# Kernel tuning notes

Measured on AMD Instinct MI355X. Metric: run time of the kernel, lower is better.

Reference implementation:

```python
import jax, jax.numpy as jnp
import numpy as np

B, S, H, L = 256, 128, 1024, 2
FEATS = {"t": 300, "v": 35, "a": 74}


def setup_inputs() -> dict:
    key = jax.random.key(0)
    inp = {}
    k = 0

    def nk():
        nonlocal k
        k += 1
        return jax.random.fold_in(key, k)

    inp["t_input"] = jax.random.normal(nk(), (B, S, FEATS["t"]), jnp.float32)
    inp["v_input"] = jax.random.normal(nk(), (B, S, FEATS["v"]), jnp.float32)
    inp["a_input"] = jax.random.normal(nk(), (B, S, FEATS["a"]), jnp.float32)
    std = 1.0 / np.sqrt(H)
    for m, f in FEATS.items():
        in_sizes = [f + 2 * H, H]  # layer0 gets modality feat + two cross-modal hiddens
        for l in range(L):
            inp[f"Wih_{m}{l}"] = jax.random.normal(nk(), (4 * H, in_sizes[l]), jnp.float32) * std
            inp[f"Whh_{m}{l}"] = jax.random.normal(nk(), (4 * H, H), jnp.float32) * std
            inp[f"bih_{m}{l}"] = jax.random.normal(nk(), (4 * H,), jnp.float32) * std
            inp[f"bhh_{m}{l}"] = jax.random.normal(nk(), (4 * H,), jnp.float32) * std
    inp["Wd"] = jax.random.normal(nk(), (1, 3 * H), jnp.float32) * np.sqrt(2.0 / (1 + 3 * H))
    inp["bd"] = jnp.zeros((1,), jnp.float32)
    return inp


def _cell(x, h, c, Wih, Whh, bih, bhh):
    # PyTorch LSTM gate order: i, f, g, o
    z = x @ Wih.T + h @ Whh.T + bih + bhh  # [B, 4H]
    i, f, g, o = jnp.split(z, 4, axis=-1)
    c_new = jax.nn.sigmoid(f) * c + jax.nn.sigmoid(i) * jnp.tanh(g)
    h_new = jax.nn.sigmoid(o) * jnp.tanh(c_new)
    return h_new, c_new


def _stack_cell(x, hs, cs, layers):
    new_h, new_c = [], []
    inp = x
    for l, (Wih, Whh, bih, bhh) in enumerate(layers):
        h, c = _cell(inp, hs[l], cs[l], Wih, Whh, bih, bhh)
        new_h.append(h)
        new_c.append(c)
        inp = h
    return jnp.stack(new_h), jnp.stack(new_c)


def _forward(t_input, v_input, a_input, pt, pv, pa, Wd, bd):
    z = jnp.zeros((L, B, H), t_input.dtype)
    carry0 = (z, z, z, z, z, z)
    xs = (t_input.transpose(1, 0, 2), v_input.transpose(1, 0, 2), a_input.transpose(1, 0, 2))

    def step(carry, x):
        ht, ct, hv, cv, ha, ca = carry
        xt, xv, xa = x
        tf, vf, af = ht[-1], hv[-1], ha[-1]  # top-layer hiddens from previous step
        t_in = jnp.concatenate([xt, vf, af], axis=-1)
        v_in = jnp.concatenate([xv, tf, af], axis=-1)
        a_in = jnp.concatenate([xa, tf, vf], axis=-1)
        ht, ct = _stack_cell(t_in, ht, ct, pt)
        hv, cv = _stack_cell(v_in, hv, cv, pv)
        ha, ca = _stack_cell(a_in, ha, ca, pa)
        return (ht, ct, hv, cv, ha, ca), None

    (ht, ct, hv, cv, ha, ca), _ = jax.lax.scan(step, carry0, xs)
    feat = jnp.concatenate([ht[-1], hv[-1], ha[-1]], axis=-1)  # [B, 3H]
    return feat @ Wd.T + bd  # [B, 1]


def reference(t_input, v_input, a_input,
              Wih_t0, Whh_t0, bih_t0, bhh_t0, Wih_t1, Whh_t1, bih_t1, bhh_t1,
              Wih_v0, Whh_v0, bih_v0, bhh_v0, Wih_v1, Whh_v1, bih_v1, bhh_v1,
              Wih_a0, Whh_a0, bih_a0, bhh_a0, Wih_a1, Whh_a1, bih_a1, bhh_a1,
              Wd, bd):
    pt = [(Wih_t0, Whh_t0, bih_t0, bhh_t0), (Wih_t1, Whh_t1, bih_t1, bhh_t1)]
    pv = [(Wih_v0, Whh_v0, bih_v0, bhh_v0), (Wih_v1, Whh_v1, bih_v1, bhh_v1)]
    pa = [(Wih_a0, Whh_a0, bih_a0, bhh_a0), (Wih_a1, Whh_a1, bih_a1, bhh_a1)]
    return _forward(t_input, v_input, a_input, pt, pv, pa, Wd, bd)
```

## Files before the change

### kernel.cpp

```cpp
#include <hip/hip_runtime.h>
#include <hip/hip_fp16.h>
#include <cstdint>
#include <cstddef>


typedef _Float16 half8 __attribute__((ext_vector_type(8)));
typedef float floatx4 __attribute__((ext_vector_type(4)));

__device__ __forceinline__ void gload16(const void* g, void* l) {
  __builtin_amdgcn_global_load_lds(
      (const __attribute__((address_space(1))) void*)g,
      (__attribute__((address_space(3))) void*)l, 16, 0, 0);
}
__device__ __forceinline__ float fsig(float x) {
  return 1.f / (1.f + __expf(-x));
}
__device__ __forceinline__ float ftanhf(float x) {
  x = fminf(15.f, fmaxf(-15.f, x));
  float e = __expf(2.f * x);
  return (e - 1.f) / (e + 1.f);
}

struct ModParam {
  const __half* xseg;
  const __half* inseg;
  const __half* W;
  const float* bias;
  float* c;
  __half* dst0; __half* dst1; __half* dst2;
  int off0, off1, off2;
  __half* feat; int featoff;
  int Kx, Kin;
};
struct PhaseParams { ModParam m[3]; };

__global__ __launch_bounds__(256, 3) void lstm_phase(PhaseParams P) {
  const int b_ = blockIdx.x;
  const int xcd = b_ & 7, rnd = b_ >> 3;
  const int pairIdx = xcd * 24 + (rnd >> 2);
  const int mt = rnd & 3;
  const int mod = pairIdx >> 6;
  const int bn = pairIdx & 63;
  const ModParam p = P.m[mod];
  const int nKt = (p.Kx + p.Kin) >> 7;
  const int KxT = p.Kx >> 7;
  const int tid = threadIdx.x;
  const int lane = tid & 63, wid = tid >> 6;
  const int ln = lane & 15, lm = lane >> 4, c4 = lane & 3;

  __shared__ __align__(16) __half smem[3][1024][8];

  floatx4 acc[4][4];
#pragma unroll
  for (int a = 0; a < 4; ++a)
#pragma unroll
    for (int b = 0; b < 4; ++b) acc[a][b] = (floatx4)0.f;

  half8 bvA[4], bvB[4];

  auto stageA = [&](int kt, int buf) {
    const __half* base; int kq0;
    if (kt < KxT) { base = p.xseg;  kq0 = kt * 16; }
    else          { base = p.inseg; kq0 = (kt - KxT) * 16; }
#pragma unroll
    for (int it = 0; it < 4; ++it) {
      int idx = it * 256 + tid;
      int kql = idx >> 6, bl = idx & 63;
      gload16(base + ((size_t)(kq0 + kql) * 256 + mt * 64 + bl) * 8,
              &smem[buf][idx][0]);
    }
  };
  auto loadB = [&](int kt, half8 (&bv)[4]) {
    const __half* src =
        p.W + ((size_t)(bn * nKt + kt) * 4 + wid) * 2048 + lane * 8;
#pragma unroll
    for (int ni = 0; ni < 4; ++ni) bv[ni] = *(const half8*)(src + ni * 512);
  };
  auto compute = [&](int buf, const half8 (&bv)[4]) {
    half8 av[4];
    const int kq = wid * 4 + lm;
#pragma unroll
    for (int mi = 0; mi < 4; ++mi)
      av[mi] = *(const half8*)&smem[buf][kq * 64 + mi * 16 + ln][0];
#pragma unroll
    for (int mi = 0; mi < 4; ++mi)
#pragma unroll
      for (int ni = 0; ni < 4; ++ni)
        acc[mi][ni] = __builtin_amdgcn_mfma_f32_16x16x32_f16(
            av[mi], bv[ni], acc[mi][ni], 0, 0, 0);
  };

  stageA(0, 0);
  loadB(0, bvA);
  int kt = 0;
  while (true) {
    if (kt + 1 < nKt) {
      stageA(kt + 1, (kt + 1) % 3);
      loadB(kt + 1, bvB);
      asm volatile("s_waitcnt vmcnt(8)" ::: "memory");
    } else {
      asm volatile("s_waitcnt vmcnt(0)" ::: "memory");
    }
    __builtin_amdgcn_s_barrier();
    __builtin_amdgcn_sched_barrier(0);
    compute(kt % 3, bvA);
    if (++kt >= nKt) break;
    if (kt + 1 < nKt) {
      stageA(kt + 1, (kt + 1) % 3);
      loadB(kt + 1, bvA);
      asm volatile("s_waitcnt vmcnt(8)" ::: "memory");
    } else {
      asm volatile("s_waitcnt vmcnt(0)" ::: "memory");
    }
    __builtin_amdgcn_s_barrier();
    __builtin_amdgcn_sched_barrier(0);
    compute(kt % 3, bvB);
    if (++kt >= nKt) break;
  }
  __syncthreads();

  floatx4* rbuf = (floatx4*)&smem[0][0][0];
  auto slot = [&](int h, int ni, int w) {
    return ((h * 4 + ni) * 4 + w) * 64 + lane;
  };
  floatx4 own[4];
#pragma unroll
  for (int ni = 0; ni < 4; ++ni) {
    rbuf[slot(0, ni, wid)] = acc[0][ni];
    rbuf[slot(1, ni, wid)] = acc[1][ni];
  }
  __syncthreads();
  if (wid == 0) {
#pragma unroll
    for (int ni = 0; ni < 4; ++ni)
      own[ni] = acc[0][ni] + rbuf[slot(0, ni, 1)] + rbuf[slot(0, ni, 2)] +
                rbuf[slot(0, ni, 3)];
  } else if (wid == 1) {
#pragma unroll
    for (int ni = 0; ni < 4; ++ni)
      own[ni] = acc[1][ni] + rbuf[slot(1, ni, 0)] + rbuf[slot(1, ni, 2)] +
                rbuf[slot(1, ni, 3)];
  }
  __syncthreads();
#pragma unroll
  for (int ni = 0; ni < 4; ++ni) {
    rbuf[slot(0, ni, wid)] = acc[2][ni];
    rbuf[slot(1, ni, wid)] = acc[3][ni];
  }
  __syncthreads();
  if (wid == 2) {
#pragma unroll
    for (int ni = 0; ni < 4; ++ni)
      own[ni] = acc[2][ni] + rbuf[slot(0, ni, 0)] + rbuf[slot(0, ni, 1)] +
                rbuf[slot(0, ni, 3)];
  } else if (wid == 3) {
#pragma unroll
    for (int ni = 0; ni < 4; ++ni)
      own[ni] = acc[3][ni] + rbuf[slot(1, ni, 0)] + rbuf[slot(1, ni, 1)] +
                rbuf[slot(1, ni, 2)];
  }

#pragma unroll
  for (int ni = 0; ni < 4; ++ni) {
    const int ncol = bn * 64 + ni * 16 + ln;
    const float bia = p.bias[ncol];
    const int j = ncol >> 2;
#pragma unroll
    for (int r = 0; r < 4; ++r) {
      float v = own[ni][r] + bia;
      float g1 = __shfl_xor(v, 1);
      float g2 = __shfl_xor(v, 2);
      float g3 = __shfl_xor(v, 3);
      int m0 = c4, m1 = c4 ^ 1, m2 = c4 ^ 2, m3 = c4 ^ 3;
      float zi = m0 == 0 ? v : (m0 == 1 ? g1 : (m0 == 2 ? g2 : g3));
      float zf = m1 == 0 ? v : (m1 == 1 ? g1 : (m1 == 2 ? g2 : g3));
      float zg = m2 == 0 ? v : (m2 == 1 ? g1 : (m2 == 2 ? g2 : g3));
      float zo = m3 == 0 ? v : (m3 == 1 ? g1 : (m3 == 2 ? g2 : g3));
      const int b = mt * 64 + wid * 16 + lm * 4 + r;
      float cp = p.c[b * 1024 + j];
      float cn = fsig(zf) * cp + fsig(zi) * ftanhf(zg);
      float hn = fsig(zo) * ftanhf(cn);
      __half h16 = __float2half(hn);
      if (c4 == 0) {
        if (p.dst0) {
          int col = p.off0 + j;
          p.dst0[(size_t)(col >> 3) * 2048 + b * 8 + (col & 7)] = h16;
        }
      } else if (c4 == 1) {
        if (p.dst1) {
          int col = p.off1 + j;
          p.dst1[(size_t)(col >> 3) * 2048 + b * 8 + (col & 7)] = h16;
        }
      } else if (c4 == 2) {
        if (p.dst2) {
          int col = p.off2 + j;
          p.dst2[(size_t)(col >> 3) * 2048 + b * 8 + (col & 7)] = h16;
        }
      } else {
        p.c[b * 1024 + j] = cn;
        if (p.feat) p.feat[(size_t)b * 3072 + p.featoff + j] = h16;
      }
    }
  }
}

__global__ void pack_w(__half* dst, const float* Wih, const float* Whh,
                       float* bdst, const float* bih, const float* bhh,
                       int f, int fpad, int hih, int Ktot) {
  long long i = (long long)blockIdx.x * 256 + threadIdx.x;
  long long tot = (long long)4096 * Ktot;
  const int nKt = Ktot >> 7;
  if (i < tot) {
    int q = (int)(i >> 11);
    int wid = q & 3;
    int p2 = q >> 2;
    int ktile = p2 % nKt, nt = p2 / nKt;
    int r = (int)(i & 2047);
    int ni = r >> 9, lane = (r >> 3) & 63, e = r & 7;
    int n = nt * 64 + ni * 16 + (lane & 15);
    int nsrc = (n & 3) * 1024 + (n >> 2);
    int k = ktile * 128 + wid * 32 + (lane >> 4) * 8 + e;
    float v;
    if (k < fpad)
      v = (k < f) ? Wih[(size_t)nsrc * (f + hih) + k] : 0.f;
    else if (k < fpad + hih)
      v = Wih[(size_t)nsrc * (f + hih) + f + (k - fpad)];
    else
      v = Whh[(size_t)nsrc * 1024 + (k - fpad - hih)];
    dst[i] = __float2half(v);
  }
  if (i < 4096) {
    int nsrc = ((int)i & 3) * 1024 + ((int)i >> 2);
    bdst[i] = bih[nsrc] + bhh[nsrc];
  }
}

__global__ void pack_x(__half* dst, const float* x, int f, int fpad) {
  long long i = (long long)blockIdx.x * 256 + threadIdx.x;
  long long tot = (long long)128 * 256 * fpad;
  if (i >= tot) return;
  int e = (int)(i & 7);
  long long u = i >> 3;
  int b = (int)(u & 255);
  long long v = u >> 8;
  int nq = fpad >> 3;
  int kq = (int)(v % nq);
  int t = (int)(v / nq);
  int k = kq * 8 + e;
  dst[i] = (k < f) ? __float2half(x[((size_t)b * 128 + t) * f + k])
                   : __float2half(0.f);
}

__global__ void final_dot(const __half* feat, const float* Wd, const float* bd,
                          float* out) {
  int b = blockIdx.x, tid = threadIdx.x;
  float s = 0.f;
  for (int j = tid; j < 3072; j += 256)
    s += __half2float(feat[(size_t)b * 3072 + j]) * Wd[j];
  __shared__ float red[256];
  red[tid] = s;
  __syncthreads();
  for (int o = 128; o > 0; o >>= 1) {
    if (tid < o) red[tid] += red[tid + o];
    __syncthreads();
  }
  if (tid == 0) out[b] = red[0] + bd[0];
}

extern "C" void kernel_launch(void* const* d_in, const int* in_sizes, int n_in,
                              void* d_out, int out_size, void* d_ws, size_t ws_size,
                              hipStream_t stream) {
  const int B = 256, S = 128, H = 1024, NG = 4096;
  const int FRAW[3] = {300, 35, 74};
  const int FPAD[3] = {384, 128, 128};

  const float* xin[3] = {(const float*)d_in[0], (const float*)d_in[1],
                         (const float*)d_in[2]};
  const float *Wih0[3], *Whh0[3], *bih0[3], *bhh0[3];
  const float *Wih1[3], *Whh1[3], *bih1[3], *bhh1[3];
  for (int m = 0; m < 3; ++m) {
    int bidx = 3 + m * 8;
    Wih0[m] = (const float*)d_in[bidx + 0];
    Whh0[m] = (const float*)d_in[bidx + 1];
    bih0[m] = (const float*)d_in[bidx + 2];
    bhh0[m] = (const float*)d_in[bidx + 3];
    Wih1[m] = (const float*)d_in[bidx + 4];
    Whh1[m] = (const float*)d_in[bidx + 5];
    bih1[m] = (const float*)d_in[bidx + 6];
    bhh1[m] = (const float*)d_in[bidx + 7];
  }
  const float* Wd = (const float*)d_in[27];
  const float* bd = (const float*)d_in[28];

  uint8_t* wsb = (uint8_t*)d_ws;
  size_t off = 0;
  auto alloc = [&](size_t bytes) -> void* {
    void* p = wsb + off;
    off += (bytes + 255) & ~(size_t)255;
    return p;
  };

  __half* W0[3];
  __half* W1[3];
  int K0[3];
  for (int m = 0; m < 3; ++m) {
    K0[m] = FPAD[m] + 3 * H;
    W0[m] = (__half*)alloc((size_t)NG * K0[m] * 2);
  }
  for (int m = 0; m < 3; ++m) W1[m] = (__half*)alloc((size_t)NG * 2 * H * 2);
  float* biasB = (float*)alloc((size_t)6 * NG * 4);
  __half* X16[3];
  for (int m = 0; m < 3; ++m)
    X16[m] = (__half*)alloc((size_t)S * B * FPAD[m] * 2);
  size_t stateStart = off;
  __half* In0[3];
  __half* In1[3];
  for (int m = 0; m < 3; ++m) In0[m] = (__half*)alloc((size_t)2 * B * 3072 * 2);
  for (int m = 0; m < 3; ++m) In1[m] = (__half*)alloc((size_t)2 * B * 2048 * 2);
  float* cbuf = (float*)alloc((size_t)6 * B * H * 4);
  size_t stateEnd = off;
  __half* featB = (__half*)alloc((size_t)B * 3072 * 2);

  if (off > ws_size) return;

  for (int m = 0; m < 3; ++m) {
    long long tot0 = (long long)NG * K0[m];
    pack_w<<<dim3((unsigned)((tot0 + 255) / 256)), 256, 0, stream>>>(
        W0[m], Wih0[m], Whh0[m], biasB + m * NG, bih0[m], bhh0[m],
        FRAW[m], FPAD[m], 2 * H, K0[m]);
    long long tot1 = (long long)NG * 2 * H;
    pack_w<<<dim3((unsigned)((tot1 + 255) / 256)), 256, 0, stream>>>(
        W1[m], Wih1[m], Whh1[m], biasB + (3 + m) * NG, bih1[m], bhh1[m],
        0, 0, H, 2 * H);
    long long totx = (long long)S * B * FPAD[m];
    pack_x<<<dim3((unsigned)((totx + 255) / 256)), 256, 0, stream>>>(
        X16[m], xin[m], FRAW[m], FPAD[m]);
  }
  hipMemsetAsync(wsb + stateStart, 0, stateEnd - stateStart, stream);

  for (int t = 0; t < S; ++t) {
    int pq = t & 1;
    __half* in0cur[3], *in0nxt[3], *in1cur[3], *in1nxt[3];
    for (int m = 0; m < 3; ++m) {
      in0cur[m] = In0[m] + (size_t)pq * B * 3072;
      in0nxt[m] = In0[m] + (size_t)(pq ^ 1) * B * 3072;
      in1cur[m] = In1[m] + (size_t)pq * B * 2048;
      in1nxt[m] = In1[m] + (size_t)(pq ^ 1) * B * 2048;
    }

    PhaseParams PA;
    for (int m = 0; m < 3; ++m) {
      ModParam& q = PA.m[m];
      q.xseg = X16[m] + (size_t)t * B * FPAD[m];
      q.Kx = FPAD[m];
      q.inseg = in0cur[m];
      q.Kin = 3072;
      q.W = W0[m];
      q.bias = biasB + m * NG;
      q.c = cbuf + (size_t)m * B * H;
      q.dst0 = in1cur[m]; q.off0 = 0;
      q.dst1 = in0nxt[m]; q.off1 = 2048;
      q.dst2 = nullptr;   q.off2 = 0;
      q.feat = nullptr;   q.featoff = 0;
    }
    lstm_phase<<<dim3(768), 256, 0, stream>>>(PA);

    PhaseParams PB;
    for (int m = 0; m < 3; ++m) {
      ModParam& q = PB.m[m];
      q.xseg = nullptr; q.Kx = 0;
      q.inseg = in1cur[m]; q.Kin = 2048;
      q.W = W1[m];
      q.bias = biasB + (3 + m) * NG;
      q.c = cbuf + (size_t)(3 + m) * B * H;
      q.feat = (t == S - 1) ? featB : nullptr;
      q.featoff = m * H;
      if (m == 0) {
        q.dst0 = in0nxt[1]; q.off0 = 0;
        q.dst1 = in0nxt[2]; q.off1 = 0;
        q.dst2 = in1nxt[0]; q.off2 = 1024;
      } else if (m == 1) {
        q.dst0 = in0nxt[0]; q.off0 = 0;
        q.dst1 = in0nxt[2]; q.off1 = 1024;
        q.dst2 = in1nxt[1]; q.off2 = 1024;
      } else {
        q.dst0 = in0nxt[0]; q.off0 = 1024;
        q.dst1 = in0nxt[1]; q.off1 = 1024;
        q.dst2 = in1nxt[2]; q.off2 = 1024;
      }
    }
    lstm_phase<<<dim3(768), 256, 0, stream>>>(PB);
  }

  final_dot<<<dim3(256), 256, 0, stream>>>(featB, Wd, bd, (float*)d_out);
}
```

Baseline: 9.882 ms.

## Give each wave a private LDS A-slice and drop per-tile block barriers

Rearranges the shared-memory A tile so each wave loads, with global_load_lds, exactly the K rows it later reads. That makes the per-k-tile s_barrier unnecessary, since waves no longer consume data written by other waves. It also prefetches A two tiles ahead, with staged vmcnt waits for the tail iterations. The intent is to stop waves stalling on each other in the GEMM main loop, in exchange for a different LDS layout (more per-wave partitioning) and more conservative wait counts that may hold back some of the extra prefetch depth.

```diff
diff --git a/kernel.cpp b/kernel.cpp
--- a/kernel.cpp
+++ b/kernel.cpp
@@ -48,7 +48,7 @@
   const int lane = tid & 63, wid = tid >> 6;
   const int ln = lane & 15, lm = lane >> 4, c4 = lane & 3;
 
-  __shared__ __align__(16) __half smem[3][1024][8];
+  __shared__ __align__(16) __half smem[4][3][2048];
 
   floatx4 acc[4][4];
 #pragma unroll
@@ -58,16 +58,14 @@
 
   half8 bvA[4], bvB[4];
 
-  auto stageA = [&](int kt, int buf) {
+  auto stageA = [&](int kt, int slot) {
     const __half* base; int kq0;
     if (kt < KxT) { base = p.xseg;  kq0 = kt * 16; }
     else          { base = p.inseg; kq0 = (kt - KxT) * 16; }
 #pragma unroll
-    for (int it = 0; it < 4; ++it) {
-      int idx = it * 256 + tid;
-      int kql = idx >> 6, bl = idx & 63;
-      gload16(base + ((size_t)(kq0 + kql) * 256 + mt * 64 + bl) * 8,
-              &smem[buf][idx][0]);
+    for (int kql = 0; kql < 4; ++kql) {
+      gload16(base + ((size_t)(kq0 + wid * 4 + kql) * 256 + mt * 64 + lane) * 8,
+              &smem[wid][slot][kql * 512 + lane * 8]);
     }
   };
   auto loadB = [&](int kt, half8 (&bv)[4]) {
@@ -76,12 +74,11 @@
 #pragma unroll
     for (int ni = 0; ni < 4; ++ni) bv[ni] = *(const half8*)(src + ni * 512);
   };
-  auto compute = [&](int buf, const half8 (&bv)[4]) {
+  auto compute = [&](int slot, const half8 (&bv)[4]) {
     half8 av[4];
-    const int kq = wid * 4 + lm;
 #pragma unroll
     for (int mi = 0; mi < 4; ++mi)
-      av[mi] = *(const half8*)&smem[buf][kq * 64 + mi * 16 + ln][0];
+      av[mi] = *(const half8*)&smem[wid][slot][lm * 512 + (mi * 16 + ln) * 8];
 #pragma unroll
     for (int mi = 0; mi < 4; ++mi)
 #pragma unroll
@@ -91,30 +88,37 @@
   };
 
   stageA(0, 0);
+  stageA(1, 1);
   loadB(0, bvA);
   int kt = 0;
   while (true) {
-    if (kt + 1 < nKt) {
-      stageA(kt + 1, (kt + 1) % 3);
-      loadB(kt + 1, bvB);
-      asm volatile("s_waitcnt vmcnt(8)" ::: "memory");
-    } else {
-      asm volatile("s_waitcnt vmcnt(0)" ::: "memory");
-    }
-    __builtin_amdgcn_s_barrier();
-    __builtin_amdgcn_sched_barrier(0);
-    compute(kt % 3, bvA);
+    {
+      if (kt + 2 < nKt) stageA(kt + 2, (kt + 2) % 3);
+      if (kt + 1 < nKt) loadB(kt + 1, bvB);
+      if (kt + 2 < nKt) {
+        asm volatile("s_waitcnt vmcnt(8)" ::: "memory");
+      } else if (kt + 1 < nKt) {
+        asm volatile("s_waitcnt vmcnt(4)" ::: "memory");
+      } else {
+        asm volatile("s_waitcnt vmcnt(0)" ::: "memory");
+      }
+      __builtin_amdgcn_sched_barrier(0);
+      compute(kt % 3, bvA);
+    }
     if (++kt >= nKt) break;
-    if (kt + 1 < nKt) {
-      stageA(kt + 1, (kt + 1) % 3);
-      loadB(kt + 1, bvA);
-      asm volatile("s_waitcnt vmcnt(8)" ::: "memory");
-    } else {
-      asm volatile("s_waitcnt vmcnt(0)" ::: "memory");
-    }
-    __builtin_amdgcn_s_barrier();
-    __builtin_amdgcn_sched_barrier(0);
-    compute(kt % 3, bvB);
+    {
+      if (kt + 2 < nKt) stageA(kt + 2, (kt + 2) % 3);
+      if (kt + 1 < nKt) loadB(kt + 1, bvA);
+      if (kt + 2 < nKt) {
+        asm volatile("s_waitcnt vmcnt(8)" ::: "memory");
+      } else if (kt + 1 < nKt) {
+        asm volatile("s_waitcnt vmcnt(4)" ::: "memory");
+      } else {
+        asm volatile("s_waitcnt vmcnt(0)" ::: "memory");
+      }
+      __builtin_amdgcn_sched_barrier(0);
+      compute(kt % 3, bvB);
+    }
     if (++kt >= nKt) break;
   }
   __syncthreads();
```

Result: no change. 9.902 ms (+0.2%).
